# Kernel optimization log

Hardware: AMD Instinct MI355X
Metric: run time of the kernel (lower is better)

Reference implementation:

```python
import jax, jax.numpy as jnp
import numpy as np

SCOPE = 63          # length of ricker inhibition filter (odd)
IN_CHANNELS = 256   # circulant matrix size == channel dim
SELF_CONNECT = False


def ricker(scope, width, damp, self_connect=False):
    # symmetric ricker (mexican-hat) wavelet of length `scope`, centered
    x = jnp.arange(scope, dtype=jnp.float32) - scope // 2
    w2 = width * width
    r = damp * (1.0 - x * x / w2) * jnp.exp(-x * x / (2.0 * w2))
    if not self_connect:
        r = r.at[scope // 2].set(0.0)  # no self-connection: zero center tap
    return r


def toeplitz1d_circular(f, size):
    # embed the centered length-`scope` filter into the first row of a
    # size x size circulant matrix (center tap on the diagonal, tails wrap)
    half = f.shape[0] // 2
    row0 = jnp.zeros(size, f.dtype)
    row0 = row0.at[: half + 1].set(f[half:])      # center + right tail
    row0 = row0.at[size - half:].set(f[:half])    # left tail wraps around
    idx = (jnp.arange(size)[:, None] - jnp.arange(size)[None, :]) % size
    return row0[idx]  # C[i, j] = row0[(i - j) mod size]


def setup_inputs() -> dict:
    key = jax.random.key(0)
    activations = jax.random.normal(key, (64, IN_CHANNELS, 56, 56), dtype=jnp.float32)
    damp = jnp.asarray(0.12, dtype=jnp.float32)   # learnable scalar
    width = jnp.asarray(3.0, dtype=jnp.float32)   # learnable scalar
    return {"activations": activations, "damp": damp, "width": width}


def reference(activations, damp, width):
    f = ricker(SCOPE, width, damp, SELF_CONNECT)
    tpl = toeplitz1d_circular(f, IN_CHANNELS)
    tpl_inv = jnp.linalg.inv(jnp.eye(IN_CHANNELS, dtype=f.dtype) - tpl)
    # apply inhibition matrix along the channel axis at every pixel
    return jnp.einsum('ij,bjhw->bihw', tpl_inv, activations)
```

## Files before the change

### kernel.cpp

```cpp
#include <hip/hip_runtime.h>


#define IN_CH 256
#define HW    3136
#define TP    64
#define KC    128

typedef _Float16 f16x8 __attribute__((ext_vector_type(8)));
typedef float    f32x4 __attribute__((ext_vector_type(4)));


__global__ __launch_bounds__(256) void pi_build(const float* __restrict__ damp,
                                                const float* __restrict__ width,
                                                f16x8* __restrict__ afrag) {
    __shared__ float cS[256], gS[256], ctab[256], mS[256];
    int t = threadIdx.x;
    float w = width[0], dmp = damp[0];

    ctab[t] = cosf((float)t * 0.0245436926f );

    int x = (t < 128) ? t : t - 256;
    float cv = 0.0f;
    if (t != 0 && x >= -31 && x <= 31) {
        float fx2 = (float)(x * x);
        float w2  = w * w;
        cv = dmp * (1.0f - fx2 / w2) * expf(-fx2 / (2.0f * w2));
    }
    cS[t] = cv;
    __syncthreads();

    float lam = 0.0f;
#pragma unroll 8
    for (int n = 0; n < 256; n++) lam += cS[n] * ctab[(t * n) & 255];
    gS[t] = 1.0f / (1.0f - lam);
    __syncthreads();

    float md = 0.0f;
#pragma unroll 8
    for (int k = 0; k < 256; k++) md += gS[k] * ctab[(t * k) & 255];
    mS[t] = md * (1.0f / 256.0f);
    __syncthreads();

#pragma unroll
    for (int g = 0; g < 32; g++) {
        int gid = g * 256 + t;
        int l  = gid & 63;
        int tt = (gid >> 6) & 15;
        int s  = gid >> 10;
        int i     = 16 * tt + (l & 15);
        int kbase = 32 * s + 8 * (l >> 4);
        f16x8 h;
#pragma unroll
        for (int j = 0; j < 8; j++)
            h[j] = (_Float16)mS[(i - (kbase + j)) & 255];
        afrag[gid] = h;
    }
}

__device__ __forceinline__ int lds_didx(int p, int cb16) {
    int cb = (cb16 ^ (p & 15) ^ ((p >> 2) & 3) ^ ((p >> 4) & 3)) & 15;
    return p * 64 + cb * 4;
}

__global__ __launch_bounds__(256, 4) void pi_gemm(const float* __restrict__ act,
                                                  float* __restrict__ out,
                                                  const f16x8* __restrict__ afrag) {
    __shared__ __align__(16) unsigned int lds[TP * KC / 2];

    int tid  = threadIdx.x;
    int lane = tid & 63;
    int wv   = tid >> 6;

    int b    = blockIdx.x / 49;
    int tile = blockIdx.x - b * 49;
    int p0   = tile * TP;

    const float* actb = act + (size_t)b * (IN_CH * HW) + p0;
    float*       outb = out + (size_t)b * (IN_CH * HW) + p0;

    f32x4 acc[4][4] = {};

    int pl = 4 * (tid & 15);
    int jb = tid >> 4;

    for (int c = 0; c < 2; c++) {
        {
            const float* src = actb + (size_t)(c * KC + jb * 8) * HW + pl;
            f32x4 v[8];
#pragma unroll
            for (int jj = 0; jj < 8; jj++)
                v[jj] = *(const f32x4*)(src + (size_t)jj * HW);
#pragma unroll
            for (int pp = 0; pp < 4; pp++) {
                int p = pl + pp;
                int didx = lds_didx(p, jb);
                f16x8 hv;
#pragma unroll
                for (int jj = 0; jj < 8; jj++)
                    hv[jj] = (_Float16)v[jj][pp];
                *(f16x8*)(lds + didx) = hv;
            }
        }
        __syncthreads();

#pragma unroll
        for (int s = 0; s < 4; s++) {
            f16x8 bh[4];
#pragma unroll
            for (int ni = 0; ni < 4; ni++) {
                int p    = 16 * ni + (lane & 15);
                int cb16 = 4 * s + (lane >> 4);
                bh[ni] = *(const f16x8*)(lds + lds_didx(p, cb16));
            }
            int sg = 4 * c + s;
#pragma unroll
            for (int ti = 0; ti < 4; ti++) {
                int t = 4 * wv + ti;
                f16x8 ah = afrag[(sg * 16 + t) * 64 + lane];
#pragma unroll
                for (int ni = 0; ni < 4; ni++)
                    acc[ti][ni] = __builtin_amdgcn_mfma_f32_16x16x32_f16(ah, bh[ni], acc[ti][ni], 0, 0, 0);
            }
        }
        __syncthreads();
    }

    int col  = lane & 15;
    int rowq = (lane >> 4) * 4;
#pragma unroll
    for (int ti = 0; ti < 4; ti++) {
        int ibase = 64 * wv + 16 * ti + rowq;
#pragma unroll
        for (int ni = 0; ni < 4; ni++) {
            int p = 16 * ni + col;
#pragma unroll
            for (int r = 0; r < 4; r++)
                outb[(size_t)(ibase + r) * HW + p] = acc[ti][ni][r];
        }
    }
}

extern "C" void kernel_launch(void* const* d_in, const int* in_sizes, int n_in,
                              void* d_out, int out_size, void* d_ws, size_t ws_size,
                              hipStream_t stream) {
    const float* act   = (const float*)d_in[0];
    const float* damp  = (const float*)d_in[1];
    const float* width = (const float*)d_in[2];
    float* out = (float*)d_out;

    f16x8* afrag = (f16x8*)d_ws;
    int batches = in_sizes[0] / (IN_CH * HW);

    pi_build<<<1, 256, 0, stream>>>(damp, width, afrag);
    pi_gemm<<<batches * 49, 256, 0, stream>>>(act, out, afrag);
}
```

Measured before the change: 371.1 us.

## Load activations straight into MFMA B-fragments, drop LDS staging, use 32x32 MFMA

New measurement: 383.3 us. 1.03x slower.

```diff
diff --git a/kernel.cpp b/kernel.cpp
--- a/kernel.cpp
+++ b/kernel.cpp
@@ -4,10 +4,9 @@
 #define IN_CH 256
 #define HW    3136
 #define TP    64
-#define KC    128
 
-typedef _Float16 f16x8 __attribute__((ext_vector_type(8)));
-typedef float    f32x4 __attribute__((ext_vector_type(4)));
+typedef _Float16 f16x8  __attribute__((ext_vector_type(8)));
+typedef float    f32x16 __attribute__((ext_vector_type(16)));
 
 
 __global__ __launch_bounds__(256) void pi_build(const float* __restrict__ damp,
@@ -45,10 +44,10 @@
     for (int g = 0; g < 32; g++) {
         int gid = g * 256 + t;
         int l  = gid & 63;
-        int tt = (gid >> 6) & 15;
-        int s  = gid >> 10;
-        int i     = 16 * tt + (l & 15);
-        int kbase = 32 * s + 8 * (l >> 4);
+        int tt = (gid >> 6) & 7;
+        int s  = gid >> 9;
+        int i     = 32 * tt + (l & 31);
+        int kbase = 16 * s + 8 * (l >> 5);
         f16x8 h;
 #pragma unroll
         for (int j = 0; j < 8; j++)
@@ -57,16 +56,35 @@
     }
 }
 
-__device__ __forceinline__ int lds_didx(int p, int cb16) {
-    int cb = (cb16 ^ (p & 15) ^ ((p >> 2) & 3) ^ ((p >> 4) & 3)) & 15;
-    return p * 64 + cb * 4;
+__device__ __forceinline__ void loads16(const float* __restrict__ src, float* v) {
+#pragma unroll
+    for (int j = 0; j < 8; j++) {
+        v[j]     = src[(size_t)j * HW];
+        v[8 + j] = src[(size_t)j * HW + 32];
+    }
+}
+
+__device__ __forceinline__ void compute16(const float* v,
+                                          const f16x8* __restrict__ afrag,
+                                          int base, int lane,
+                                          f32x16 acc[2][2]) {
+    f16x8 b0, b1;
+#pragma unroll
+    for (int j = 0; j < 8; j++) {
+        b0[j] = (_Float16)v[j];
+        b1[j] = (_Float16)v[8 + j];
+    }
+    f16x8 a0 = afrag[(base + 0) * 64 + lane];
+    f16x8 a1 = afrag[(base + 1) * 64 + lane];
+    acc[0][0] = __builtin_amdgcn_mfma_f32_32x32x16_f16(a0, b0, acc[0][0], 0, 0, 0);
+    acc[0][1] = __builtin_amdgcn_mfma_f32_32x32x16_f16(a0, b1, acc[0][1], 0, 0, 0);
+    acc[1][0] = __builtin_amdgcn_mfma_f32_32x32x16_f16(a1, b0, acc[1][0], 0, 0, 0);
+    acc[1][1] = __builtin_amdgcn_mfma_f32_32x32x16_f16(a1, b1, acc[1][1], 0, 0, 0);
 }
 
 __global__ __launch_bounds__(256, 4) void pi_gemm(const float* __restrict__ act,
                                                   float* __restrict__ out,
                                                   const f16x8* __restrict__ afrag) {
-    __shared__ __align__(16) unsigned int lds[TP * KC / 2];
-
     int tid  = threadIdx.x;
     int lane = tid & 63;
     int wv   = tid >> 6;
@@ -75,67 +93,38 @@
     int tile = blockIdx.x - b * 49;
     int p0   = tile * TP;
 
-    const float* actb = act + (size_t)b * (IN_CH * HW) + p0;
-    float*       outb = out + (size_t)b * (IN_CH * HW) + p0;
+    int col   = lane & 31;
+    int khalf = (lane >> 5) * 8;
 
-    f32x4 acc[4][4] = {};
+    const float* actb = act + (size_t)b * (IN_CH * HW) + p0 + col;
+    float*       outb = out + (size_t)b * (IN_CH * HW) + p0 + col;
 
-    int pl = 4 * (tid & 15);
-    int jb = tid >> 4;
+    f32x16 acc[2][2] = {};
 
-    for (int c = 0; c < 2; c++) {
-        {
-            const float* src = actb + (size_t)(c * KC + jb * 8) * HW + pl;
-            f32x4 v[8];
+    float v0[16], v1[16];
+    const float* ksrc = actb + (size_t)khalf * HW;
+
+    loads16(ksrc, v0);
 #pragma unroll
-            for (int jj = 0; jj < 8; jj++)
-                v[jj] = *(const f32x4*)(src + (size_t)jj * HW);
-#pragma unroll
-            for (int pp = 0; pp < 4; pp++) {
-                int p = pl + pp;
-                int didx = lds_didx(p, jb);
-                f16x8 hv;
-#pragma unroll
-                for (int jj = 0; jj < 8; jj++)
-                    hv[jj] = (_Float16)v[jj][pp];
-                *(f16x8*)(lds + didx) = hv;
-            }
-        }
-        __syncthreads();
-
-#pragma unroll
-        for (int s = 0; s < 4; s++) {
-            f16x8 bh[4];
-#pragma unroll
-            for (int ni = 0; ni < 4; ni++) {
-                int p    = 16 * ni + (lane & 15);
-                int cb16 = 4 * s + (lane >> 4);
-                bh[ni] = *(const f16x8*)(lds + lds_didx(p, cb16));
-            }
-            int sg = 4 * c + s;
-#pragma unroll
-            for (int ti = 0; ti < 4; ti++) {
-                int t = 4 * wv + ti;
-                f16x8 ah = afrag[(sg * 16 + t) * 64 + lane];
-#pragma unroll
-                for (int ni = 0; ni < 4; ni++)
-                    acc[ti][ni] = __builtin_amdgcn_mfma_f32_16x16x32_f16(ah, bh[ni], acc[ti][ni], 0, 0, 0);
-            }
-        }
-        __syncthreads();
+    for (int ss = 0; ss < 8; ss++) {
+        loads16(ksrc + (size_t)(16 * (2 * ss + 1)) * HW, v1);
+        compute16(v0, afrag, (2 * ss) * 8 + 2 * wv, lane, acc);
+        if (ss < 7)
+            loads16(ksrc + (size_t)(16 * (2 * ss + 2)) * HW, v0);
+        compute16(v1, afrag, (2 * ss + 1) * 8 + 2 * wv, lane, acc);
     }
 
-    int col  = lane & 15;
-    int rowq = (lane >> 4) * 4;
+    int rb = 4 * (lane >> 5);
 #pragma unroll
-    for (int ti = 0; ti < 4; ti++) {
-        int ibase = 64 * wv + 16 * ti + rowq;
+    for (int ti = 0; ti < 2; ti++) {
 #pragma unroll
-        for (int ni = 0; ni < 4; ni++) {
-            int p = 16 * ni + col;
+        for (int ni = 0; ni < 2; ni++) {
+            float* dst = outb + (size_t)(64 * wv + 32 * ti + rb) * HW + 32 * ni;
 #pragma unroll
-            for (int r = 0; r < 4; r++)
-                outb[(size_t)(ibase + r) * HW + p] = acc[ti][ni][r];
+            for (int r = 0; r < 16; r++) {
+                int row = (r & 3) + 8 * (r >> 2);
+                __builtin_nontemporal_store(acc[ti][ni][r], dst + (size_t)row * HW);
+            }
         }
     }
 }
```
